# Performance work log

Measured on AMD Instinct MI355X. Metric: run time of the kernel, lower is better.

Reference implementation:

```python
import jax, jax.numpy as jnp
import numpy as np

DIM = 512
HEADS = 8
DIM_HEAD = 64
INNER = HEADS * DIM_HEAD


def setup_inputs() -> dict:
    key = jax.random.key(0)
    k1, k2, k3, k4 = jax.random.split(key, 4)
    x = jax.random.normal(k1, (4, 8192, DIM), dtype=jnp.float32)
    # nn.Linear(dim, inner*3, bias=False): weight applied as x @ W^T; store transposed form [dim, 3*inner]
    w_qkv = jax.random.normal(k2, (DIM, 3 * INNER), dtype=jnp.float32) / np.sqrt(DIM)
    w_out = jax.random.normal(k3, (INNER, DIM), dtype=jnp.float32) / np.sqrt(INNER)
    b_out = jax.random.normal(k4, (DIM,), dtype=jnp.float32) * 0.01
    return {"x": x, "w_qkv": w_qkv, "w_out": w_out, "b_out": b_out}


def reference(x, w_qkv, w_out, b_out):
    b, n, d = x.shape
    qkv = x @ w_qkv  # [b, n, 3*inner]
    q, k, v = jnp.split(qkv, 3, axis=-1)

    def to_heads(t):
        return t.reshape(b, n, HEADS, DIM_HEAD).transpose(0, 2, 1, 3)  # [b,h,n,dh]

    q, k, v = map(to_heads, (q, k, v))
    q = jax.nn.elu(q) + 1.0
    k = jax.nn.elu(k) + 1.0
    # kv summary: [b,h,dh,dh]
    kv = jnp.einsum('bhnd,bhnm->bhdm', k, v)
    # normalizer z: [b,h,n]  (note: original does NOT apply self.scale)
    z = 1.0 / (jnp.einsum('bhnd,bhd->bhn', q, k.sum(axis=2)) + 1e-6)
    out = jnp.einsum('bhnd,bhdm->bhnm', q, kv) * z[..., None]  # [b,h,n,dh]
    out = out.transpose(0, 2, 1, 3).reshape(b, n, INNER)
    return out @ w_out + b_out
```

## Files before the change

### kernel.cpp

```cpp
#include <hip/hip_runtime.h>
#include <hip/hip_bf16.h>

#define B_SZ 4
#define SEQ 8192
#define DIM 512
#define HEADS 8
#define DH 64
#define INNER 512
#define QKV_COLS 1536
#define M_TOT (B_SZ * SEQ)
#define BHN (B_SZ * HEADS)

typedef __bf16 bf16x8 __attribute__((ext_vector_type(8)));
typedef __bf16 bf16x4 __attribute__((ext_vector_type(4)));
typedef float f32x4 __attribute__((ext_vector_type(4)));

__device__ __forceinline__ float elu1(float x) {
    return x > 0.f ? x + 1.f : __expf(x);
}

__device__ __forceinline__ void gl_lds16(const void* g, void* l) {
    __builtin_amdgcn_global_load_lds(
        (const __attribute__((address_space(1))) unsigned int*)g,
        (__attribute__((address_space(3))) unsigned int*)l, 16, 0, 0);
}

#define NXBLK (M_TOT * DIM / 4 / 256)
__global__ void convert_all(const float* __restrict__ x,
                            const float* __restrict__ w_qkv,
                            const float* __restrict__ w_out,
                            __bf16* __restrict__ xb,
                            __bf16* __restrict__ wqkv_t,
                            __bf16* __restrict__ wout_t) {
    int blk = blockIdx.x;
    int tid = threadIdx.x;
    if (blk < NXBLK) {
        int id = blk * 256 + tid;
        float4 f = reinterpret_cast<const float4*>(x)[id];
        bf16x4 h = {(__bf16)f.x, (__bf16)f.y, (__bf16)f.z, (__bf16)f.w};
        reinterpret_cast<bf16x4*>(xb)[id] = h;
        return;
    }
    __shared__ float T[64][65];
    int tile = blk - NXBLK;
    const float* src; __bf16* dst; int tk, tn, srcld, dstld;
    if (tile < 192) {
        src = w_qkv; dst = wqkv_t; srcld = QKV_COLS; dstld = DIM;
        tk = (tile & 7) * 64; tn = (tile >> 3) * 64;
    } else {
        tile -= 192;
        src = w_out; dst = wout_t; srcld = DIM; dstld = INNER;
        tk = (tile & 7) * 64; tn = (tile >> 3) * 64;
    }
#pragma unroll
    for (int i = 0; i < 16; ++i) {
        int idx = tid + i * 256;
        int r = idx >> 6, c = idx & 63;
        T[r][c] = src[(size_t)(tk + r) * srcld + tn + c];
    }
    __syncthreads();
#pragma unroll
    for (int i = 0; i < 16; ++i) {
        int idx = tid + i * 256;
        int r = idx >> 6, c = idx & 63;
        dst[(size_t)(tn + r) * dstld + tk + c] = (__bf16)T[c][r];
    }
}

#define TSTR 136
__launch_bounds__(256, 4)
__global__ void gemm_qkv(const __bf16* __restrict__ xb,
                         const __bf16* __restrict__ wqkv_t,
                         __bf16* __restrict__ q_ws,
                         __bf16* __restrict__ kT_ws,
                         __bf16* __restrict__ vT_ws) {
    __shared__ __attribute__((aligned(16))) char smem[128 * TSTR * 2];
    __bf16* As = (__bf16*)smem;
    __bf16* Bs = (__bf16*)(smem + 16384);
    __bf16* T  = (__bf16*)smem;

    const int tid = threadIdx.x;
    const int wid = tid >> 6;
    const int lane = tid & 63;
    const int wm = wid >> 1, wn = wid & 1;
    const int lq = lane >> 4, lr = lane & 15;
    const int m0 = blockIdx.x * 128;
    const int n0 = blockIdx.y * 128;
    const int lrow = lane >> 3;
    const int lsw  = ((lane & 7) ^ lrow) * 8;

    f32x4 acc[4][4] = {};

    for (int kb = 0; kb < DIM; kb += 64) {
#pragma unroll
        for (int t = 0; t < 4; ++t) {
            int qi = wid * 4 + t;
            int row = qi * 8 + lrow;
            gl_lds16(&xb[(size_t)(m0 + row) * DIM + kb + lsw], &As[qi * 512]);
            gl_lds16(&wqkv_t[(size_t)(n0 + row) * DIM + kb + lsw], &Bs[qi * 512]);
        }
        __syncthreads();
#pragma unroll
        for (int ks = 0; ks < 2; ++ks) {
            const int csw = ((ks * 4 + lq) ^ (lr & 7)) * 8;
            bf16x8 af[4], bfv[4];
#pragma unroll
            for (int i = 0; i < 4; ++i)
                af[i] = *reinterpret_cast<const bf16x8*>(
                    &As[(wm * 64 + i * 16 + lr) * 64 + csw]);
#pragma unroll
            for (int j = 0; j < 4; ++j)
                bfv[j] = *reinterpret_cast<const bf16x8*>(
                    &Bs[(wn * 64 + j * 16 + lr) * 64 + csw]);
#pragma unroll
            for (int i = 0; i < 4; ++i)
#pragma unroll
                for (int j = 0; j < 4; ++j)
                    acc[i][j] = __builtin_amdgcn_mfma_f32_16x16x32_bf16(
                        af[i], bfv[j], acc[i][j], 0, 0, 0);
        }
        __syncthreads();
    }

    const int which = n0 / INNER;
    const int n0w = n0 % INNER;
    const int b = m0 / SEQ;
    const int nbase = m0 % SEQ;

    if (which == 0) {
#pragma unroll
        for (int i = 0; i < 4; ++i)
#pragma unroll
            for (int j = 0; j < 4; ++j) {
                int col = wn * 64 + j * 16 + lr;
#pragma unroll
                for (int r = 0; r < 4; ++r)
                    T[(wm * 64 + i * 16 + lq * 4 + r) * TSTR + col] =
                        (__bf16)elu1(acc[i][j][r]);
            }
        __syncthreads();
#pragma unroll
        for (int it = 0; it < 8; ++it) {
            int c = tid + it * 256;
            int row = c >> 4, dc = (c & 15) * 8;
            bf16x8 v = *reinterpret_cast<const bf16x8*>(&T[row * TSTR + dc]);
            int col = n0w + dc;
            int h = col >> 6, d = col & 63;
            *reinterpret_cast<bf16x8*>(
                &q_ws[(((size_t)(b * HEADS + h)) * SEQ + nbase + row) * DH + d]) = v;
        }
    } else {
        __bf16* dst = (which == 1) ? kT_ws : vT_ws;
#pragma unroll
        for (int i = 0; i < 4; ++i)
#pragma unroll
            for (int j = 0; j < 4; ++j) {
                int col = wn * 64 + j * 16 + lr;
                int rowb = wm * 64 + i * 16 + lq * 4;
                bf16x4 h4;
#pragma unroll
                for (int r = 0; r < 4; ++r) {
                    float v = acc[i][j][r];
                    h4[r] = (__bf16)((which == 1) ? elu1(v) : v);
                }
                *reinterpret_cast<bf16x4*>(&T[col * TSTR + rowb]) = h4;
            }
        __syncthreads();
#pragma unroll
        for (int it = 0; it < 8; ++it) {
            int c = tid + it * 256;
            int colIdx = c >> 4, rc = (c & 15) * 8;
            bf16x8 v = *reinterpret_cast<const bf16x8*>(&T[colIdx * TSTR + rc]);
            int gcol = n0w + colIdx;
            int h = gcol >> 6, d = gcol & 63;
            *reinterpret_cast<bf16x8*>(
                &dst[(((size_t)(b * HEADS + h)) * DH + d) * SEQ + nbase + rc]) = v;
        }
    }
}

__launch_bounds__(256, 4)
__global__ void kv_reduce(const __bf16* __restrict__ kT,
                          const __bf16* __restrict__ vT,
                          float* __restrict__ kv_t,
                          float* __restrict__ ksum) {
    __shared__ __attribute__((aligned(16))) __bf16 Ks[64][136];
    __shared__ __attribute__((aligned(16))) __bf16 Vs[64][136];
    const int tid = threadIdx.x;
    const int wid = tid >> 6;
    const int lane = tid & 63;
    const int lq = lane >> 4, lr = lane & 15;
    const int bh = blockIdx.y;
    const int n0 = blockIdx.x * 256;
    const size_t base = (size_t)bh * DH * SEQ;
    f32x4 acc[4] = {};
    f32x4 acc1 = {};
    bf16x8 ones8;
#pragma unroll
    for (int e = 0; e < 8; ++e) ones8[e] = (__bf16)1.f;

    for (int ch = 0; ch < 2; ++ch) {
        int nc = n0 + ch * 128;
#pragma unroll
        for (int t = 0; t < 4; ++t) {
            int c = tid + t * 256;
            int row = c >> 4, kc = (c & 15) * 8;
            *reinterpret_cast<bf16x8*>(&Ks[row][kc]) =
                *reinterpret_cast<const bf16x8*>(&kT[base + (size_t)row * SEQ + nc + kc]);
            *reinterpret_cast<bf16x8*>(&Vs[row][kc]) =
                *reinterpret_cast<const bf16x8*>(&vT[base + (size_t)row * SEQ + nc + kc]);
        }
        __syncthreads();
#pragma unroll
        for (int ks = 0; ks < 4; ++ks) {
            bf16x8 a = *reinterpret_cast<const bf16x8*>(&Ks[wid * 16 + lr][ks * 32 + lq * 8]);
            acc1 = __builtin_amdgcn_mfma_f32_16x16x32_bf16(a, ones8, acc1, 0, 0, 0);
#pragma unroll
            for (int j = 0; j < 4; ++j) {
                bf16x8 b = *reinterpret_cast<const bf16x8*>(&Vs[j * 16 + lr][ks * 32 + lq * 8]);
                acc[j] = __builtin_amdgcn_mfma_f32_16x16x32_bf16(a, b, acc[j], 0, 0, 0);
            }
        }
        __syncthreads();
    }
    float* dst = kv_t + (size_t)bh * DH * DH;
#pragma unroll
    for (int j = 0; j < 4; ++j) {
        int m = j * 16 + lr;
#pragma unroll
        for (int r = 0; r < 4; ++r) {
            int d = wid * 16 + lq * 4 + r;
            atomicAdd(&dst[m * DH + d], acc[j][r]);
        }
    }
    if (lr == 0) {
#pragma unroll
        for (int r = 0; r < 4; ++r)
            atomicAdd(&ksum[bh * DH + wid * 16 + lq * 4 + r], acc1[r]);
    }
}

__launch_bounds__(256, 4)
__global__ void attn_kernel(const __bf16* __restrict__ q_ws,
                            const float* __restrict__ kv_t,
                            const float* __restrict__ ksum,
                            __bf16* __restrict__ attn) {
    __shared__ __attribute__((aligned(16))) __bf16 Qs[128][72];
    __shared__ __attribute__((aligned(16))) __bf16 KVs[64][72];
    __shared__ float zs[128];
    __shared__ float ks_s[64];
    const int tid = threadIdx.x;
    const int wid = tid >> 6, lane = tid & 63;
    const int lq = lane >> 4, lr = lane & 15;
    const int bh = blockIdx.y;
    const int b = bh >> 3, h = bh & 7;
    const int n0 = blockIdx.x * 128;
    const size_t qbase = ((size_t)bh * SEQ + n0) * DH;

#pragma unroll
    for (int t = 0; t < 4; ++t) {
        int c = tid + t * 256;
        int row = c >> 3, kc = (c & 7) * 8;
        *reinterpret_cast<bf16x8*>(&Qs[row][kc]) =
            *reinterpret_cast<const bf16x8*>(&q_ws[qbase + (size_t)row * DH + kc]);
    }
    const float* kvsrc = kv_t + (size_t)bh * DH * DH;
#pragma unroll
    for (int t = 0; t < 4; ++t) {
        int c = tid + t * 256;
        int m = c >> 4, dc = (c & 15) * 4;
        float4 f = *reinterpret_cast<const float4*>(&kvsrc[m * DH + dc]);
        bf16x4 h4 = {(__bf16)f.x, (__bf16)f.y, (__bf16)f.z, (__bf16)f.w};
        *reinterpret_cast<bf16x4*>(&KVs[m][dc]) = h4;
    }
    if (tid < 64) ks_s[tid] = ksum[bh * DH + tid];
    __syncthreads();
    {
        int row = tid >> 1, part = tid & 1;
        float s = 0.f;
#pragma unroll
        for (int jj = 0; jj < 4; ++jj) {
            bf16x8 qv = *reinterpret_cast<const bf16x8*>(&Qs[row][part * 32 + jj * 8]);
#pragma unroll
            for (int e = 0; e < 8; ++e)
                s += (float)qv[e] * ks_s[part * 32 + jj * 8 + e];
        }
        s += __shfl_xor(s, 1, 64);
        if (part == 0) zs[row] = 1.f / (s + 1e-6f);
    }
    __syncthreads();

    f32x4 acc[2][4] = {};
#pragma unroll
    for (int ks = 0; ks < 2; ++ks) {
        bf16x8 a0 = *reinterpret_cast<const bf16x8*>(&Qs[wid * 32 + lr][ks * 32 + lq * 8]);
        bf16x8 a1 = *reinterpret_cast<const bf16x8*>(&Qs[wid * 32 + 16 + lr][ks * 32 + lq * 8]);
#pragma unroll
        for (int j = 0; j < 4; ++j) {
            bf16x8 bfr = *reinterpret_cast<const bf16x8*>(&KVs[j * 16 + lr][ks * 32 + lq * 8]);
            acc[0][j] = __builtin_amdgcn_mfma_f32_16x16x32_bf16(a0, bfr, acc[0][j], 0, 0, 0);
            acc[1][j] = __builtin_amdgcn_mfma_f32_16x16x32_bf16(a1, bfr, acc[1][j], 0, 0, 0);
        }
    }
    __syncthreads();
#pragma unroll
    for (int mt = 0; mt < 2; ++mt)
#pragma unroll
        for (int j = 0; j < 4; ++j) {
            int m = j * 16 + lr;
#pragma unroll
            for (int r = 0; r < 4; ++r) {
                int row = wid * 32 + mt * 16 + lq * 4 + r;
                Qs[row][m] = (__bf16)(acc[mt][j][r] * zs[row]);
            }
        }
    __syncthreads();
#pragma unroll
    for (int it = 0; it < 4; ++it) {
        int c = tid + it * 256;
        int row = c >> 3, mc = (c & 7) * 8;
        bf16x8 v = *reinterpret_cast<const bf16x8*>(&Qs[row][mc]);
        *reinterpret_cast<bf16x8*>(
            &attn[((size_t)(b * SEQ + n0 + row)) * INNER + h * DH + mc]) = v;
    }
}

__launch_bounds__(256, 4)
__global__ void gemm_out(const __bf16* __restrict__ attn,
                         const __bf16* __restrict__ wout_t,
                         const float* __restrict__ b_out,
                         float* __restrict__ out) {
    __shared__ __attribute__((aligned(16))) char smem[32768];
    __bf16* As = (__bf16*)smem;
    __bf16* Bs = (__bf16*)(smem + 16384);

    const int tid = threadIdx.x;
    const int wid = tid >> 6;
    const int lane = tid & 63;
    const int wm = wid >> 1, wn = wid & 1;
    const int lq = lane >> 4, lr = lane & 15;
    const int m0 = blockIdx.x * 128;
    const int n0 = blockIdx.y * 128;
    const int lrow = lane >> 3;
    const int lsw  = ((lane & 7) ^ lrow) * 8;

    f32x4 acc[4][4] = {};

    for (int kb = 0; kb < INNER; kb += 64) {
#pragma unroll
        for (int t = 0; t < 4; ++t) {
            int qi = wid * 4 + t;
            int row = qi * 8 + lrow;
            gl_lds16(&attn[(size_t)(m0 + row) * INNER + kb + lsw], &As[qi * 512]);
            gl_lds16(&wout_t[(size_t)(n0 + row) * INNER + kb + lsw], &Bs[qi * 512]);
        }
        __syncthreads();
#pragma unroll
        for (int ks = 0; ks < 2; ++ks) {
            const int csw = ((ks * 4 + lq) ^ (lr & 7)) * 8;
            bf16x8 af[4], bfv[4];
#pragma unroll
            for (int i = 0; i < 4; ++i)
                af[i] = *reinterpret_cast<const bf16x8*>(
                    &As[(wm * 64 + i * 16 + lr) * 64 + csw]);
#pragma unroll
            for (int j = 0; j < 4; ++j)
                bfv[j] = *reinterpret_cast<const bf16x8*>(
                    &Bs[(wn * 64 + j * 16 + lr) * 64 + csw]);
#pragma unroll
            for (int i = 0; i < 4; ++i)
#pragma unroll
                for (int j = 0; j < 4; ++j)
                    acc[i][j] = __builtin_amdgcn_mfma_f32_16x16x32_bf16(
                        af[i], bfv[j], acc[i][j], 0, 0, 0);
        }
        __syncthreads();
    }

#pragma unroll
    for (int j = 0; j < 4; ++j) {
        int col = n0 + wn * 64 + j * 16 + lr;
        float bias = b_out[col];
#pragma unroll
        for (int i = 0; i < 4; ++i) {
            int row = m0 + wm * 64 + i * 16 + lq * 4;
#pragma unroll
            for (int r = 0; r < 4; ++r)
                out[(size_t)(row + r) * DIM + col] = acc[i][j][r] + bias;
        }
    }
}

extern "C" void kernel_launch(void* const* d_in, const int* in_sizes, int n_in,
                              void* d_out, int out_size, void* d_ws, size_t ws_size,
                              hipStream_t stream) {
    (void)in_sizes; (void)n_in; (void)out_size; (void)ws_size;
    const float* x     = (const float*)d_in[0];
    const float* w_qkv = (const float*)d_in[1];
    const float* w_out = (const float*)d_in[2];
    const float* b_out = (const float*)d_in[3];
    float* out = (float*)d_out;

    char* ws = (char*)d_ws;
    size_t off = 0;
    auto alloc = [&](size_t bytes) {
        char* p = ws + off;
        off += (bytes + 255) & ~(size_t)255;
        return p;
    };
    __bf16* xb     = (__bf16*)alloc((size_t)M_TOT * DIM * 2);
    __bf16* attn   = xb;
    __bf16* q_ws   = (__bf16*)alloc((size_t)BHN * SEQ * DH * 2);
    __bf16* kT_ws  = (__bf16*)alloc((size_t)BHN * SEQ * DH * 2);
    __bf16* vT_ws  = (__bf16*)alloc((size_t)BHN * SEQ * DH * 2);
    float*  kv_t   = (float*)alloc((size_t)BHN * DH * DH * 4 + (size_t)BHN * DH * 4);
    float*  ksum   = kv_t + (size_t)BHN * DH * DH;
    __bf16* wqkv_t = (__bf16*)alloc((size_t)QKV_COLS * DIM * 2);
    __bf16* wout_t = (__bf16*)alloc((size_t)INNER * DIM * 2);

    hipMemsetAsync(kv_t, 0, (size_t)BHN * DH * DH * 4 + (size_t)BHN * DH * 4, stream);
    convert_all<<<dim3(NXBLK + 256), 256, 0, stream>>>(
        x, w_qkv, w_out, xb, wqkv_t, wout_t);
    gemm_qkv<<<dim3(M_TOT / 128, QKV_COLS / 128), 256, 0, stream>>>(
        xb, wqkv_t, q_ws, kT_ws, vT_ws);
    kv_reduce<<<dim3(32, BHN), 256, 0, stream>>>(kT_ws, vT_ws, kv_t, ksum);
    attn_kernel<<<dim3(SEQ / 128, BHN), 256, 0, stream>>>(q_ws, kv_t, ksum, attn);
    gemm_out<<<dim3(M_TOT / 128, DIM / 128), 256, 0, stream>>>(attn, wout_t, b_out, out);
}
```

Measured before the change: 309.4 us.

## Fold kv summary into output weights and drop attention kernel

```diff
diff --git a/kernel.cpp b/kernel.cpp
--- a/kernel.cpp
+++ b/kernel.cpp
@@ -68,7 +68,7 @@
 }
 
 #define TSTR 136
-__launch_bounds__(256, 4)
+__launch_bounds__(256, 2)
 __global__ void gemm_qkv(const __bf16* __restrict__ xb,
                          const __bf16* __restrict__ wqkv_t,
                          __bf16* __restrict__ q_ws,
@@ -179,7 +179,7 @@
     }
 }
 
-__launch_bounds__(256, 4)
+__launch_bounds__(256, 2)
 __global__ void kv_reduce(const __bf16* __restrict__ kT,
                           const __bf16* __restrict__ vT,
                           float* __restrict__ kv_t,
@@ -191,7 +191,7 @@
     const int lane = tid & 63;
     const int lq = lane >> 4, lr = lane & 15;
     const int bh = blockIdx.y;
-    const int n0 = blockIdx.x * 256;
+    const int n0 = blockIdx.x * 512;
     const size_t base = (size_t)bh * DH * SEQ;
     f32x4 acc[4] = {};
     f32x4 acc1 = {};
@@ -199,7 +199,7 @@
 #pragma unroll
     for (int e = 0; e < 8; ++e) ones8[e] = (__bf16)1.f;
 
-    for (int ch = 0; ch < 2; ++ch) {
+    for (int ch = 0; ch < 4; ++ch) {
         int nc = n0 + ch * 128;
 #pragma unroll
         for (int t = 0; t < 4; ++t) {
@@ -240,96 +240,89 @@
     }
 }
 
-__launch_bounds__(256, 4)
-__global__ void attn_kernel(const __bf16* __restrict__ q_ws,
-                            const float* __restrict__ kv_t,
-                            const float* __restrict__ ksum,
-                            __bf16* __restrict__ attn) {
-    __shared__ __attribute__((aligned(16))) __bf16 Qs[128][72];
-    __shared__ __attribute__((aligned(16))) __bf16 KVs[64][72];
-    __shared__ float zs[128];
-    __shared__ float ks_s[64];
+__global__ void w2_kernel(const float* __restrict__ kv_t,
+                          const __bf16* __restrict__ wout_t,
+                          __bf16* __restrict__ w2) {
+    __shared__ __bf16 KvT[64][72];
     const int tid = threadIdx.x;
     const int wid = tid >> 6, lane = tid & 63;
     const int lq = lane >> 4, lr = lane & 15;
+    const int bh = blockIdx.x;
+    const int h = bh & 7;
+    const float* src = kv_t + (size_t)bh * DH * DH;
+
+#pragma unroll
+    for (int t = 0; t < 4; ++t) {
+        int idx = tid + t * 256;
+        float4 f = *reinterpret_cast<const float4*>(&src[idx * 4]);
+        int m = idx >> 4, d0 = (idx & 15) * 4;
+        KvT[d0 + 0][m] = (__bf16)f.x;
+        KvT[d0 + 1][m] = (__bf16)f.y;
+        KvT[d0 + 2][m] = (__bf16)f.z;
+        KvT[d0 + 3][m] = (__bf16)f.w;
+    }
+    __syncthreads();
+
+    f32x4 acc[4][8] = {};
+#pragma unroll
+    for (int ks = 0; ks < 2; ++ks) {
+        bf16x8 af[4];
+#pragma unroll
+        for (int dt = 0; dt < 4; ++dt)
+            af[dt] = *reinterpret_cast<const bf16x8*>(&KvT[dt * 16 + lr][ks * 32 + lq * 8]);
+#pragma unroll
+        for (int cj = 0; cj < 8; ++cj) {
+            bf16x8 bf = *reinterpret_cast<const bf16x8*>(
+                &wout_t[(size_t)(wid * 128 + cj * 16 + lr) * INNER + h * 64 + ks * 32 + lq * 8]);
+#pragma unroll
+            for (int dt = 0; dt < 4; ++dt)
+                acc[dt][cj] = __builtin_amdgcn_mfma_f32_16x16x32_bf16(af[dt], bf, acc[dt][cj], 0, 0, 0);
+        }
+    }
+#pragma unroll
+    for (int dt = 0; dt < 4; ++dt)
+#pragma unroll
+        for (int cj = 0; cj < 8; ++cj) {
+            int c = wid * 128 + cj * 16 + lr;
+            bf16x4 h4;
+#pragma unroll
+            for (int r = 0; r < 4; ++r) h4[r] = (__bf16)acc[dt][cj][r];
+            *reinterpret_cast<bf16x4*>(
+                &w2[((size_t)bh * 512 + c) * DH + dt * 16 + lq * 4]) = h4;
+        }
+}
+
+__global__ void qscale(__bf16* __restrict__ q_ws, const float* __restrict__ ksum) {
+    __shared__ float ks_s[DH];
+    const int tid = threadIdx.x;
     const int bh = blockIdx.y;
-    const int b = bh >> 3, h = bh & 7;
-    const int n0 = blockIdx.x * 128;
-    const size_t qbase = ((size_t)bh * SEQ + n0) * DH;
-
-#pragma unroll
-    for (int t = 0; t < 4; ++t) {
-        int c = tid + t * 256;
-        int row = c >> 3, kc = (c & 7) * 8;
-        *reinterpret_cast<bf16x8*>(&Qs[row][kc]) =
-            *reinterpret_cast<const bf16x8*>(&q_ws[qbase + (size_t)row * DH + kc]);
-    }
-    const float* kvsrc = kv_t + (size_t)bh * DH * DH;
-#pragma unroll
-    for (int t = 0; t < 4; ++t) {
-        int c = tid + t * 256;
-        int m = c >> 4, dc = (c & 15) * 4;
-        float4 f = *reinterpret_cast<const float4*>(&kvsrc[m * DH + dc]);
-        bf16x4 h4 = {(__bf16)f.x, (__bf16)f.y, (__bf16)f.z, (__bf16)f.w};
-        *reinterpret_cast<bf16x4*>(&KVs[m][dc]) = h4;
-    }
-    if (tid < 64) ks_s[tid] = ksum[bh * DH + tid];
+    if (tid < DH) ks_s[tid] = ksum[bh * DH + tid];
     __syncthreads();
-    {
-        int row = tid >> 1, part = tid & 1;
-        float s = 0.f;
-#pragma unroll
-        for (int jj = 0; jj < 4; ++jj) {
-            bf16x8 qv = *reinterpret_cast<const bf16x8*>(&Qs[row][part * 32 + jj * 8]);
-#pragma unroll
-            for (int e = 0; e < 8; ++e)
-                s += (float)qv[e] * ks_s[part * 32 + jj * 8 + e];
-        }
-        s += __shfl_xor(s, 1, 64);
-        if (part == 0) zs[row] = 1.f / (s + 1e-6f);
-    }
-    __syncthreads();
-
-    f32x4 acc[2][4] = {};
-#pragma unroll
-    for (int ks = 0; ks < 2; ++ks) {
-        bf16x8 a0 = *reinterpret_cast<const bf16x8*>(&Qs[wid * 32 + lr][ks * 32 + lq * 8]);
-        bf16x8 a1 = *reinterpret_cast<const bf16x8*>(&Qs[wid * 32 + 16 + lr][ks * 32 + lq * 8]);
-#pragma unroll
-        for (int j = 0; j < 4; ++j) {
-            bf16x8 bfr = *reinterpret_cast<const bf16x8*>(&KVs[j * 16 + lr][ks * 32 + lq * 8]);
-            acc[0][j] = __builtin_amdgcn_mfma_f32_16x16x32_bf16(a0, bfr, acc[0][j], 0, 0, 0);
-            acc[1][j] = __builtin_amdgcn_mfma_f32_16x16x32_bf16(a1, bfr, acc[1][j], 0, 0, 0);
-        }
-    }
-    __syncthreads();
-#pragma unroll
-    for (int mt = 0; mt < 2; ++mt)
-#pragma unroll
-        for (int j = 0; j < 4; ++j) {
-            int m = j * 16 + lr;
-#pragma unroll
-            for (int r = 0; r < 4; ++r) {
-                int row = wid * 32 + mt * 16 + lq * 4 + r;
-                Qs[row][m] = (__bf16)(acc[mt][j][r] * zs[row]);
-            }
-        }
-    __syncthreads();
-#pragma unroll
-    for (int it = 0; it < 4; ++it) {
-        int c = tid + it * 256;
-        int row = c >> 3, mc = (c & 7) * 8;
-        bf16x8 v = *reinterpret_cast<const bf16x8*>(&Qs[row][mc]);
-        *reinterpret_cast<bf16x8*>(
-            &attn[((size_t)(b * SEQ + n0 + row)) * INNER + h * DH + mc]) = v;
-    }
-}
-
-__launch_bounds__(256, 4)
-__global__ void gemm_out(const __bf16* __restrict__ attn,
-                         const __bf16* __restrict__ wout_t,
-                         const float* __restrict__ b_out,
-                         float* __restrict__ out) {
+    const int n = blockIdx.x * 256 + tid;
+    __bf16* row = q_ws + ((size_t)bh * SEQ + n) * DH;
+    bf16x8 v[8];
+    float s = 0.f;
+#pragma unroll
+    for (int t = 0; t < 8; ++t) {
+        v[t] = *reinterpret_cast<const bf16x8*>(&row[t * 8]);
+#pragma unroll
+        for (int e = 0; e < 8; ++e) s += (float)v[t][e] * ks_s[t * 8 + e];
+    }
+    float z = 1.f / (s + 1e-6f);
+#pragma unroll
+    for (int t = 0; t < 8; ++t) {
+        bf16x8 o;
+#pragma unroll
+        for (int e = 0; e < 8; ++e) o[e] = (__bf16)((float)v[t][e] * z);
+        *reinterpret_cast<bf16x8*>(&row[t * 8]) = o;
+    }
+}
+
+__launch_bounds__(256, 2)
+__global__ void gemm_out_fused(const __bf16* __restrict__ qp,
+                               const __bf16* __restrict__ w2,
+                               const float* __restrict__ b_out,
+                               float* __restrict__ out) {
     __shared__ __attribute__((aligned(16))) char smem[32768];
     __bf16* As = (__bf16*)smem;
     __bf16* Bs = (__bf16*)(smem + 16384);
@@ -340,19 +333,23 @@
     const int wm = wid >> 1, wn = wid & 1;
     const int lq = lane >> 4, lr = lane & 15;
     const int m0 = blockIdx.x * 128;
-    const int n0 = blockIdx.y * 128;
+    const int c0 = blockIdx.y * 128;
+    const int b = m0 / SEQ;
+    const int nbase = m0 % SEQ;
     const int lrow = lane >> 3;
     const int lsw  = ((lane & 7) ^ lrow) * 8;
 
     f32x4 acc[4][4] = {};
 
-    for (int kb = 0; kb < INNER; kb += 64) {
+    for (int h = 0; h < HEADS; ++h) {
+        const size_t abase = ((size_t)(b * HEADS + h) * SEQ + nbase) * DH;
+        const size_t bbase = ((size_t)(b * HEADS + h) * 512 + c0) * DH;
 #pragma unroll
         for (int t = 0; t < 4; ++t) {
             int qi = wid * 4 + t;
             int row = qi * 8 + lrow;
-            gl_lds16(&attn[(size_t)(m0 + row) * INNER + kb + lsw], &As[qi * 512]);
-            gl_lds16(&wout_t[(size_t)(n0 + row) * INNER + kb + lsw], &Bs[qi * 512]);
+            gl_lds16(&qp[abase + (size_t)row * DH + lsw], &As[qi * 512]);
+            gl_lds16(&w2[bbase + (size_t)row * DH + lsw], &Bs[qi * 512]);
         }
         __syncthreads();
 #pragma unroll
@@ -379,7 +376,7 @@
 
 #pragma unroll
     for (int j = 0; j < 4; ++j) {
-        int col = n0 + wn * 64 + j * 16 + lr;
+        int col = c0 + wn * 64 + j * 16 + lr;
         float bias = b_out[col];
 #pragma unroll
         for (int i = 0; i < 4; ++i) {
@@ -409,7 +406,6 @@
         return p;
     };
     __bf16* xb     = (__bf16*)alloc((size_t)M_TOT * DIM * 2);
-    __bf16* attn   = xb;
     __bf16* q_ws   = (__bf16*)alloc((size_t)BHN * SEQ * DH * 2);
     __bf16* kT_ws  = (__bf16*)alloc((size_t)BHN * SEQ * DH * 2);
     __bf16* vT_ws  = (__bf16*)alloc((size_t)BHN * SEQ * DH * 2);
@@ -417,13 +413,16 @@
     float*  ksum   = kv_t + (size_t)BHN * DH * DH;
     __bf16* wqkv_t = (__bf16*)alloc((size_t)QKV_COLS * DIM * 2);
     __bf16* wout_t = (__bf16*)alloc((size_t)INNER * DIM * 2);
+    __bf16* w2     = (__bf16*)alloc((size_t)BHN * 512 * DH * 2);
 
     hipMemsetAsync(kv_t, 0, (size_t)BHN * DH * DH * 4 + (size_t)BHN * DH * 4, stream);
     convert_all<<<dim3(NXBLK + 256), 256, 0, stream>>>(
         x, w_qkv, w_out, xb, wqkv_t, wout_t);
     gemm_qkv<<<dim3(M_TOT / 128, QKV_COLS / 128), 256, 0, stream>>>(
         xb, wqkv_t, q_ws, kT_ws, vT_ws);
-    kv_reduce<<<dim3(32, BHN), 256, 0, stream>>>(kT_ws, vT_ws, kv_t, ksum);
-    attn_kernel<<<dim3(SEQ / 128, BHN), 256, 0, stream>>>(q_ws, kv_t, ksum, attn);
-    gemm_out<<<dim3(M_TOT / 128, DIM / 128), 256, 0, stream>>>(attn, wout_t, b_out, out);
-}
+    kv_reduce<<<dim3(16, BHN), 256, 0, stream>>>(kT_ws, vT_ws, kv_t, ksum);
+    w2_kernel<<<dim3(BHN), 256, 0, stream>>>(kv_t, wout_t, w2);
+    qscale<<<dim3(SEQ / 256, BHN), 256, 0, stream>>>(q_ws, ksum);
+    gemm_out_fused<<<dim3(M_TOT / 128, DIM / 128), 256, 0, stream>>>(
+        q_ws, w2, b_out, out);
+}
```

After: 303.3 us. -2.0%, faster.
